# Kernel tuning notes

Measured on AMD Instinct MI355X. Metric: run time of the kernel, lower is better.

Reference implementation:

```python
import jax, jax.numpy as jnp
import numpy as np

EMBED = 768
FFN = 3072
HEADS = 12
HEAD_DIM = EMBED // HEADS
B, T = 4, 2048


def _layer_norm(x, g, b, eps=1e-5):
    m = jnp.mean(x, axis=-1, keepdims=True)
    v = jnp.mean((x - m) ** 2, axis=-1, keepdims=True)
    return (x - m) * jax.lax.rsqrt(v + eps) * g + b


def setup_inputs() -> dict:
    key = jax.random.key(0)
    ks = jax.random.split(key, 8)
    s_e = 1.0 / np.sqrt(EMBED)
    s_f = 1.0 / np.sqrt(FFN)
    # weights stored [in, out] (transpose of torch Linear layout)
    return {
        "x": jax.random.normal(ks[0], (B, T, EMBED), dtype=jnp.float32),
        "ln1_g": jnp.ones((EMBED,), jnp.float32),
        "ln1_b": jnp.zeros((EMBED,), jnp.float32),
        "wq": jax.random.uniform(ks[1], (EMBED, EMBED), jnp.float32, -s_e, s_e),
        "bq": jnp.zeros((EMBED,), jnp.float32),
        "wk": jax.random.uniform(ks[2], (EMBED, EMBED), jnp.float32, -s_e, s_e),
        "bk": jnp.zeros((EMBED,), jnp.float32),
        "wv": jax.random.uniform(ks[3], (EMBED, EMBED), jnp.float32, -s_e, s_e),
        "bv": jnp.zeros((EMBED,), jnp.float32),
        "wo": jax.random.uniform(ks[4], (EMBED, EMBED), jnp.float32, -s_e, s_e),
        "bo": jnp.zeros((EMBED,), jnp.float32),
        "ln2_g": jnp.ones((EMBED,), jnp.float32),
        "ln2_b": jnp.zeros((EMBED,), jnp.float32),
        "w1": jax.random.uniform(ks[5], (EMBED, FFN), jnp.float32, -s_e, s_e),
        "b1": jnp.zeros((FFN,), jnp.float32),
        "w2": jax.random.uniform(ks[6], (FFN, EMBED), jnp.float32, -s_f, s_f),
        "b2": jnp.zeros((EMBED,), jnp.float32),
    }


def reference(x, ln1_g, ln1_b, wq, bq, wk, bk, wv, bv, wo, bo,
              ln2_g, ln2_b, w1, b1, w2, b2):
    Bx, Tx, C = x.shape
    # --- self-attention block (pre-norm) ---
    residual = x
    h = _layer_norm(x, ln1_g, ln1_b)
    q = (h @ wq + bq).reshape(Bx, Tx, HEADS, HEAD_DIM)
    k = (h @ wk + bk).reshape(Bx, Tx, HEADS, HEAD_DIM)
    v = (h @ wv + bv).reshape(Bx, Tx, HEADS, HEAD_DIM)
    scale = 1.0 / np.sqrt(HEAD_DIM)
    attn = jnp.einsum('bqhd,bkhd->bhqk', q, k) * scale  # [B,H,T,T]
    attn = jax.nn.softmax(attn, axis=-1)
    o = jnp.einsum('bhqk,bkhd->bqhd', attn, v).reshape(Bx, Tx, C)
    x = residual + (o @ wo + bo)
    # --- FFN block (pre-norm) ---
    residual = x
    h = _layer_norm(x, ln2_g, ln2_b)
    h = jax.nn.gelu(h @ w1 + b1, approximate=False)
    x = residual + (h @ w2 + b2)
    return x
```

## Files before the change

kernel.cpp:

```cpp
#include <hip/hip_runtime.h>
#include <hip/hip_bf16.h>

#define EMBED 768
#define FFNDIM 3072
#define HEADS 12
#define HDIM  64
#define BB    4
#define TT    2048
#define MTOK  (BB*TT)

typedef __hip_bfloat16 bf16;
typedef __attribute__((ext_vector_type(8))) short short8;
typedef __attribute__((ext_vector_type(4))) float f32x4;
typedef __attribute__((ext_vector_type(16))) float f32x16;
typedef __attribute__((ext_vector_type(4))) unsigned short ushort4v;

__device__ __forceinline__ f32x4 mfma16(short8 a, short8 b, f32x4 c) {
  return __builtin_amdgcn_mfma_f32_16x16x32_bf16(a, b, c, 0, 0, 0);
}
__device__ __forceinline__ f32x16 mfma32(short8 a, short8 b, f32x16 c) {
  return __builtin_amdgcn_mfma_f32_32x32x16_bf16(a, b, c, 0, 0, 0);
}

__device__ __forceinline__ unsigned short f2bf(float f) {
  union { float f; unsigned int u; } v; v.f = f;
  unsigned int u = v.u;
  return (unsigned short)((u + 0x7fffu + ((u >> 16) & 1u)) >> 16);
}

__device__ __forceinline__ float fexp2(float x) {
#if __has_builtin(__builtin_amdgcn_exp2f)
  return __builtin_amdgcn_exp2f(x);
#else
  return exp2f(x);
#endif
}

__device__ __forceinline__ unsigned cvtpk(float lo, float hi) {
  unsigned r;
  asm("v_cvt_pk_bf16_f32 %0, %1, %2" : "=v"(r) : "v"(lo), "v"(hi));
  return r;
}
__device__ __forceinline__ void pl32swap(unsigned& vdst, unsigned& vsrc) {
  asm("v_permlane32_swap_b32 %0, %1" : "+v"(vdst), "+v"(vsrc));
}

__device__ __forceinline__ void gl_lds16(const void* g, void* l) {
  __builtin_amdgcn_global_load_lds((const __attribute__((address_space(1))) void*)g,
                                   (__attribute__((address_space(3))) void*)l, 16, 0, 0);
}

template <int N>
__device__ __forceinline__ void wait_vm() {
  asm volatile("s_waitcnt vmcnt(%0)" :: "i"(N) : "memory");
  __builtin_amdgcn_sched_barrier(0);
}
__device__ __forceinline__ void block_barrier() {
  __builtin_amdgcn_sched_barrier(0);
  __builtin_amdgcn_s_barrier();
  __builtin_amdgcn_sched_barrier(0);
}

#define QSCALE 0.18033688011112042f
#define DEFER_THR 11.54f

struct TArgs {
  const float* src[6];
  bf16* dst[6];
  int K[6];
  int N[6];
};

__global__ __launch_bounds__(256) void transpose_k(TArgs ta) {
  const int mi = blockIdx.z;
  const int K = ta.K[mi], N = ta.N[mi];
  const int nt = N / 32;
  const int bx = blockIdx.x % nt, by = blockIdx.x / nt;
  const int n0 = bx * 32, k0 = by * 32;
  if (k0 >= K) return;
  __shared__ float t[32][33];
  const float* __restrict__ W = ta.src[mi];
  bf16* __restrict__ Wt = ta.dst[mi];
  const int tx = threadIdx.x & 31, ty = threadIdx.x >> 5;
#pragma unroll
  for (int i = 0; i < 4; ++i) {
    int kk = ty + i * 8;
    t[tx][kk] = W[(size_t)(k0 + kk) * N + n0 + tx];
  }
  __syncthreads();
#pragma unroll
  for (int i = 0; i < 4; ++i) {
    int nn = ty + i * 8;
    Wt[(size_t)(n0 + nn) * K + k0 + tx] = __float2bfloat16(t[nn][tx]);
  }
}

__global__ __launch_bounds__(256) void ln_k(const float* __restrict__ x,
                                            const float* __restrict__ g,
                                            const float* __restrict__ b,
                                            bf16* __restrict__ out) {
  const int row = blockIdx.x * 4 + (threadIdx.x >> 6);
  const int lane = threadIdx.x & 63;
  const float* xr = x + (size_t)row * EMBED;
  float4 v[3];
  float s = 0.f;
#pragma unroll
  for (int i = 0; i < 3; ++i) {
    v[i] = *(const float4*)&xr[i * 256 + lane * 4];
    s += v[i].x + v[i].y + v[i].z + v[i].w;
  }
#pragma unroll
  for (int m = 1; m < 64; m <<= 1) s += __shfl_xor(s, m);
  const float mean = s * (1.f / 768.f);
  float ss = 0.f;
#pragma unroll
  for (int i = 0; i < 3; ++i) {
    float dx = v[i].x - mean, dy = v[i].y - mean, dz = v[i].z - mean, dw = v[i].w - mean;
    ss += dx * dx + dy * dy + dz * dz + dw * dw;
  }
#pragma unroll
  for (int m = 1; m < 64; m <<= 1) ss += __shfl_xor(ss, m);
  const float rstd = rsqrtf(ss * (1.f / 768.f) + 1e-5f);
#pragma unroll
  for (int i = 0; i < 3; ++i) {
    float4 g4 = *(const float4*)&g[i * 256 + lane * 4];
    float4 b4 = *(const float4*)&b[i * 256 + lane * 4];
    ushort4v o4;
    o4[0] = f2bf((v[i].x - mean) * rstd * g4.x + b4.x);
    o4[1] = f2bf((v[i].y - mean) * rstd * g4.y + b4.y);
    o4[2] = f2bf((v[i].z - mean) * rstd * g4.z + b4.z);
    o4[3] = f2bf((v[i].w - mean) * rstd * g4.w + b4.w);
    *(ushort4v*)&out[(size_t)row * EMBED + i * 256 + lane * 4] = o4;
  }
}

template <int EPI, int TN>
__global__ __launch_bounds__(256) void gemm_bt_k(
    const bf16* __restrict__ A, const bf16* __restrict__ Bt,
    const float* __restrict__ bias, const float* __restrict__ bias2,
    const float* __restrict__ bias3, const float* __restrict__ resid,
    float* __restrict__ outf, bf16* __restrict__ outb,
    bf16* __restrict__ outk, bf16* __restrict__ outvt,
    int N, int K) {
  constexpr int MI = (TN == 128) ? 4 : 2;
  constexpr int SN = (TN == 128) ? 4 : 3;
  const int tid = threadIdx.x;
  const int lane = tid & 63;
  const int w = tid >> 6;
  const int l16 = lane & 15, g = lane >> 4;
  const int wrbase = (TN == 128) ? (w >> 1) * 64 : w * 32;
  const int wcbase = (TN == 128) ? (w & 1) * 64 : 0;

  const int nbx = N / TN;
  const int logical = ((int)blockIdx.x & 7) * ((int)gridDim.x >> 3) + ((int)blockIdx.x >> 3);
  const int m0 = (logical / nbx) * 128, n0 = (logical % nbx) * TN;

  __shared__ bf16 Al[3][128 * 32];
  __shared__ bf16 Bl[3][TN * 32];

  f32x4 acc[MI][4];
#pragma unroll
  for (int i = 0; i < MI; ++i)
#pragma unroll
    for (int j = 0; j < 4; ++j) acc[i][j] = {0.f, 0.f, 0.f, 0.f};

  const int st_r = lane >> 2;
  const int st_c = ((lane & 3) ^ ((lane >> 3) & 3)) * 8;
  const size_t a_base = (size_t)(m0 + w * 32) * K;
  const size_t b_base = (TN == 128) ? (size_t)(n0 + w * 32) * K
                                    : (size_t)(n0 + w * 16) * K;

  auto stage = [&](int bufi, int kt) {
#pragma unroll
    for (int p = 0; p < 2; ++p)
      gl_lds16(A + a_base + (size_t)(p * 16 + st_r) * K + kt + st_c,
               &Al[bufi][(w * 32 + p * 16) * 32]);
    if constexpr (TN == 128) {
#pragma unroll
      for (int p = 0; p < 2; ++p)
        gl_lds16(Bt + b_base + (size_t)(p * 16 + st_r) * K + kt + st_c,
                 &Bl[bufi][(w * 32 + p * 16) * 32]);
    } else {
      gl_lds16(Bt + b_base + (size_t)st_r * K + kt + st_c, &Bl[bufi][(w * 16) * 32]);
    }
  };

  const int nt = K >> 5;
  stage(0, 0);
  stage(1, 32);
  const int sw = (l16 >> 1) & 3;
  int buf = 0;
  for (int t = 0; t < nt; ++t) {
    if (t < nt - 1) wait_vm<SN>(); else wait_vm<0>();
    block_barrier();
    if (t + 2 < nt) {
      int nb = buf + 2; if (nb >= 3) nb -= 3;
      stage(nb, (t + 2) * 32);
    }
    short8 af[MI], bfr[4];
#pragma unroll
    for (int i = 0; i < MI; ++i)
      af[i] = *(const short8*)&Al[buf][(wrbase + i * 16 + l16) * 32 + (g ^ sw) * 8];
#pragma unroll
    for (int j = 0; j < 4; ++j)
      bfr[j] = *(const short8*)&Bl[buf][(wcbase + j * 16 + l16) * 32 + (g ^ sw) * 8];
#pragma unroll
    for (int i = 0; i < MI; ++i)
#pragma unroll
      for (int j = 0; j < 4; ++j) acc[i][j] = mfma16(af[i], bfr[j], acc[i][j]);
    buf = (buf == 2) ? 0 : buf + 1;
  }

  const int crow = m0 + wrbase + g * 4;
  const int ccol = n0 + wcbase + l16;

  if constexpr (EPI == 0) {
    const int region = n0 / EMBED;
    const float* bp = (region == 0) ? bias : (region == 1) ? bias2 : bias3;
    if (region < 2) {
      const float sc = (region == 0) ? QSCALE : 1.0f;
      bf16* __restrict__ dst = (region == 0) ? outb : outk;
#pragma unroll
      for (int j = 0; j < 4; ++j) {
        const int cn = ccol - region * EMBED + j * 16;
        const float bvv = bp[cn];
#pragma unroll
        for (int i = 0; i < MI; ++i)
#pragma unroll
          for (int rr = 0; rr < 4; ++rr) {
            const int m = crow + i * 16 + rr;
            dst[(size_t)m * EMBED + cn] = __float2bfloat16((acc[i][j][rr] + bvv) * sc);
          }
      }
    } else {
#pragma unroll
      for (int j = 0; j < 4; ++j) {
        const int cn = ccol - 2 * EMBED + j * 16;
        const float bvv = bp[cn];
        const int hh = cn >> 6, dd = cn & 63;
#pragma unroll
        for (int i = 0; i < MI; ++i) {
          const int m = crow + i * 16;
          const int bb2 = m >> 11, t = m & 2047;
          ushort4v pk;
#pragma unroll
          for (int rr = 0; rr < 4; ++rr) pk[rr] = f2bf(acc[i][j][rr] + bvv);
          *(ushort4v*)&outvt[((size_t)((bb2 * HEADS + hh) * HDIM + dd)) * TT + t] = pk;
        }
      }
    }
  } else if constexpr (EPI == 1) {
#pragma unroll
    for (int j = 0; j < 4; ++j) {
      const int cn = ccol + j * 16;
      const float bvv = bias[cn];
#pragma unroll
      for (int i = 0; i < MI; ++i)
#pragma unroll
        for (int rr = 0; rr < 4; ++rr) {
          const int m = crow + i * 16 + rr;
          const size_t idx = (size_t)m * N + cn;
          outf[idx] = resid[idx] + acc[i][j][rr] + bvv;
        }
    }
  } else {
#pragma unroll
    for (int j = 0; j < 4; ++j) {
      const int cn = ccol + j * 16;
      const float bvv = bias[cn];
#pragma unroll
      for (int i = 0; i < MI; ++i)
#pragma unroll
        for (int rr = 0; rr < 4; ++rr) {
          const int m = crow + i * 16 + rr;
          const float v = acc[i][j][rr] + bvv;
          const float ge = 0.5f * v * (1.f + erff(v * 0.70710678118f));
          outb[(size_t)m * N + cn] = __float2bfloat16(ge);
        }
    }
  }
}

__global__ __launch_bounds__(256) void flash6_k(const bf16* __restrict__ q,
                                                const bf16* __restrict__ k,
                                                const bf16* __restrict__ vt,
                                                bf16* __restrict__ o) {
  const int tid = threadIdx.x, lane = tid & 63;
  const int l32 = lane & 31, hl = lane >> 5;
  const int w = tid >> 6;
  const int logical = ((int)blockIdx.x & 7) * 96 + ((int)blockIdx.x >> 3);
  const int qt = logical & 15;
  const int hb = logical >> 4;
  const int h = hb % HEADS, b = hb / HEADS;
  const int q0 = (qt * 4 + w) * 32;

  __shared__ bf16 Kl[3][64 * 64];
  __shared__ bf16 Vl[3][64 * 64];

  short8 qf[4];
  {
    const bf16* qp = q + (size_t)(b * TT + q0 + l32) * EMBED + h * HDIM + hl * 8;
#pragma unroll
    for (int c = 0; c < 4; ++c) qf[c] = *(const short8*)&qp[c * 16];
  }

  const bf16* __restrict__ kgs = k + (size_t)(b * TT) * EMBED + h * HDIM;
  const bf16* __restrict__ vgs = vt + ((size_t)((b * HEADS + h) * HDIM)) * TT;

  f32x16 oacc0, oacc1;
#pragma unroll
  for (int i = 0; i < 16; ++i) { oacc0[i] = 0.f; oacc1[i] = 0.f; }
  float mrun = -1.0e30f, lrun = 0.f;

  const int st_rw = w * 8 + (lane >> 3);
  const int st_cs0 = lane & 7;
  auto stage = [&](int buf, int kv) {
#pragma unroll
    for (int p = 0; p < 2; ++p) {
      const int r = p * 32 + st_rw;
      const int cs = st_cs0 ^ (r & 7);
      char* kdst = (char*)&Kl[buf][0] + p * 4096 + w * 1024;
      char* vdst = (char*)&Vl[buf][0] + p * 4096 + w * 1024;
      gl_lds16(kgs + (size_t)(kv + r) * EMBED + cs * 8, kdst);
      gl_lds16(vgs + (size_t)r * TT + kv + cs * 8, vdst);
    }
  };

  auto subtile = [&](int buf, int s2) {
    const int krow = s2 * 32 + l32;
    const char* Kb = (const char*)&Kl[buf][0];
    const char* Vb = (const char*)&Vl[buf][0];
    short8 kf[4];
#pragma unroll
    for (int c = 0; c < 4; ++c)
      kf[c] = *(const short8*)(Kb + krow * 128 + (((2 * c + hl) ^ (krow & 7)) * 16));

    f32x16 s;
#pragma unroll
    for (int i = 0; i < 16; ++i) s[i] = 0.f;
    __builtin_amdgcn_s_setprio(1);
#pragma unroll
    for (int c = 0; c < 4; ++c) s = mfma32(kf[c], qf[c], s);
    __builtin_amdgcn_s_setprio(0);

    short8 vf[4];
#pragma unroll
    for (int ks = 0; ks < 2; ++ks)
#pragma unroll
      for (int dc = 0; dc < 2; ++dc) {
        const int vrow = dc * 32 + l32;
        vf[ks * 2 + dc] = *(const short8*)(
            Vb + vrow * 128 + (((s2 * 4 + ks * 2 + hl) ^ (vrow & 7)) * 16));
      }

    float m0 = fmaxf(fmaxf(s[0], s[1]), s[2]);
    float m1 = fmaxf(fmaxf(s[3], s[4]), s[5]);
    float m2 = fmaxf(fmaxf(s[6], s[7]), s[8]);
    float m3 = fmaxf(fmaxf(s[9], s[10]), s[11]);
    float m4 = fmaxf(fmaxf(s[12], s[13]), s[14]);
    float mx = fmaxf(fmaxf(fmaxf(m0, m1), fmaxf(m2, m3)), fmaxf(m4, s[15]));
    mx = fmaxf(mx, __shfl_xor(mx, 32));

    if (!__all(mx <= mrun + DEFER_THR)) {
      const float mn = fmaxf(mrun, mx);
      const float al = fexp2(mrun - mn);
      lrun *= al;
#pragma unroll
      for (int i = 0; i < 16; ++i) { oacc0[i] *= al; oacc1[i] *= al; }
      mrun = mn;
    }

    float p[16];
#pragma unroll
    for (int i = 0; i < 16; ++i) p[i] = fexp2(s[i] - mrun);
    float a8[8];
#pragma unroll
    for (int i = 0; i < 8; ++i) a8[i] = p[2 * i] + p[2 * i + 1];
    float ps = ((a8[0] + a8[1]) + (a8[2] + a8[3])) + ((a8[4] + a8[5]) + (a8[6] + a8[7]));
    ps += __shfl_xor(ps, 32);
    lrun += ps;

    union { unsigned u[4]; short8 s8; } pa0, pa1;
    {
      unsigned U = cvtpk(p[0], p[1]), V = cvtpk(p[4], p[5]);
      pl32swap(V, U); pa0.u[0] = U; pa0.u[2] = V;
      unsigned U1 = cvtpk(p[2], p[3]), V1 = cvtpk(p[6], p[7]);
      pl32swap(V1, U1); pa0.u[1] = U1; pa0.u[3] = V1;
    }
    {
      unsigned U = cvtpk(p[8], p[9]), V = cvtpk(p[12], p[13]);
      pl32swap(V, U); pa1.u[0] = U; pa1.u[2] = V;
      unsigned U1 = cvtpk(p[10], p[11]), V1 = cvtpk(p[14], p[15]);
      pl32swap(V1, U1); pa1.u[1] = U1; pa1.u[3] = V1;
    }

    __builtin_amdgcn_s_setprio(1);
    oacc0 = mfma32(vf[0], pa0.s8, oacc0);
    oacc0 = mfma32(vf[2], pa1.s8, oacc0);
    oacc1 = mfma32(vf[1], pa0.s8, oacc1);
    oacc1 = mfma32(vf[3], pa1.s8, oacc1);
    __builtin_amdgcn_s_setprio(0);
  };

  const int NT = TT / 64;
  stage(0, 0);
  stage(1, 64);
  int buf = 0;
  for (int t = 0; t < NT; ++t) {
    if (t < NT - 1) wait_vm<4>(); else wait_vm<0>();
    block_barrier();
    if (t + 2 < NT) {
      int nb = buf + 2; if (nb >= 3) nb -= 3;
      stage(nb, (t + 2) * 64);
    }
    subtile(buf, 0);
    subtile(buf, 1);
    buf = (buf == 2) ? 0 : buf + 1;
  }

  const float inv = 1.f / lrun;
  bf16* op = o + (size_t)(b * TT + q0 + l32) * EMBED + h * HDIM;
#pragma unroll
  for (int a = 0; a < 4; ++a) {
    ushort4v pk4;
#pragma unroll
    for (int bb = 0; bb < 4; ++bb) pk4[bb] = f2bf(oacc0[a * 4 + bb] * inv);
    *(ushort4v*)&op[a * 8 + hl * 4] = pk4;
#pragma unroll
    for (int bb = 0; bb < 4; ++bb) pk4[bb] = f2bf(oacc1[a * 4 + bb] * inv);
    *(ushort4v*)&op[32 + a * 8 + hl * 4] = pk4;
  }
}

extern "C" void kernel_launch(void* const* d_in, const int* in_sizes, int n_in,
                              void* d_out, int out_size, void* d_ws,
                              size_t ws_size, hipStream_t stream) {
  const float* x = (const float*)d_in[0];
  const float* ln1g = (const float*)d_in[1];
  const float* ln1b = (const float*)d_in[2];
  const float* wq = (const float*)d_in[3];
  const float* bq = (const float*)d_in[4];
  const float* wk = (const float*)d_in[5];
  const float* bk = (const float*)d_in[6];
  const float* wv = (const float*)d_in[7];
  const float* bv = (const float*)d_in[8];
  const float* wo = (const float*)d_in[9];
  const float* bo = (const float*)d_in[10];
  const float* ln2g = (const float*)d_in[11];
  const float* ln2b = (const float*)d_in[12];
  const float* w1 = (const float*)d_in[13];
  const float* b1 = (const float*)d_in[14];
  const float* w2 = (const float*)d_in[15];
  const float* b2 = (const float*)d_in[16];
  float* out = (float*)d_out;

  char* ws = (char*)d_ws;
  size_t off = 0;
  auto alloc = [&](size_t bytes) {
    char* p = ws + off;
    off += (bytes + 255) & ~(size_t)255;
    return p;
  };
  bf16* wqkv_t = (bf16*)alloc((size_t)2304 * 768 * 2);
  bf16* wo_t = (bf16*)alloc((size_t)768 * 768 * 2);
  bf16* w1_t = (bf16*)alloc((size_t)3072 * 768 * 2);
  bf16* w2_t = (bf16*)alloc((size_t)768 * 3072 * 2);
  bf16* h = (bf16*)alloc((size_t)MTOK * EMBED * 2);
  char* qkvo = alloc((size_t)MTOK * EMBED * 2 * 4);
  bf16* qb = (bf16*)qkvo;
  bf16* kb = qb + (size_t)MTOK * EMBED;
  bf16* vtb = kb + (size_t)MTOK * EMBED;
  bf16* ob = vtb + (size_t)MTOK * EMBED;
  bf16* h1 = (bf16*)qkvo;
  float* x1 = (float*)alloc((size_t)MTOK * EMBED * 4);
  (void)ws_size;

  TArgs ta;
  ta.src[0] = wq; ta.dst[0] = wqkv_t;                  ta.K[0] = 768;  ta.N[0] = 768;
  ta.src[1] = wk; ta.dst[1] = wqkv_t + 768 * 768;      ta.K[1] = 768;  ta.N[1] = 768;
  ta.src[2] = wv; ta.dst[2] = wqkv_t + 2 * 768 * 768;  ta.K[2] = 768;  ta.N[2] = 768;
  ta.src[3] = wo; ta.dst[3] = wo_t;                    ta.K[3] = 768;  ta.N[3] = 768;
  ta.src[4] = w1; ta.dst[4] = w1_t;                    ta.K[4] = 768;  ta.N[4] = 3072;
  ta.src[5] = w2; ta.dst[5] = w2_t;                    ta.K[5] = 3072; ta.N[5] = 768;

  transpose_k<<<dim3(2304, 1, 6), dim3(256), 0, stream>>>(ta);
  ln_k<<<dim3(MTOK / 4), dim3(256), 0, stream>>>(x, ln1g, ln1b, h);
  gemm_bt_k<0, 128><<<dim3((2304 / 128) * (MTOK / 128)), dim3(256), 0, stream>>>(
      h, wqkv_t, bq, bk, bv, nullptr, nullptr, qb, kb, vtb, 2304, 768);
  flash6_k<<<dim3(16 * HEADS * BB), dim3(256), 0, stream>>>(qb, kb, vtb, ob);
  gemm_bt_k<1, 64><<<dim3((768 / 64) * (MTOK / 128)), dim3(256), 0, stream>>>(
      ob, wo_t, bo, nullptr, nullptr, x, x1, nullptr, nullptr, nullptr, 768, 768);
  ln_k<<<dim3(MTOK / 4), dim3(256), 0, stream>>>(x1, ln2g, ln2b, h);
  gemm_bt_k<2, 128><<<dim3((3072 / 128) * (MTOK / 128)), dim3(256), 0, stream>>>(
      h, w1_t, b1, nullptr, nullptr, nullptr, nullptr, h1, nullptr, nullptr, 3072, 768);
  gemm_bt_k<1, 64><<<dim3((768 / 64) * (MTOK / 128)), dim3(256), 0, stream>>>(
      h1, w2_t, b2, nullptr, nullptr, x1, out, nullptr, nullptr, nullptr, 768, 3072);
}
```

Baseline: 314.6 us.

## Split attention KV range in two halves and merge with a combine kernel

Splits each attention query tile's KV sequence into two halves processed by separate blocks (split-K flash attention). Each block writes unnormalized bf16 partial outputs plus running max and sum, and a new combine kernel merges the two halves with rescaling. V is now read directly from global memory instead of being staged in LDS, and K staging drops from triple to double buffering with full barriers. This doubles the grid for better occupancy, at the cost of an extra kernel, extra partial-output traffic, bf16 rounding of the unnormalized partials, and uncached V loads.

```diff
diff --git a/kernel.cpp b/kernel.cpp
--- a/kernel.cpp
+++ b/kernel.cpp
@@ -281,21 +281,24 @@
   }
 }
 
-__global__ __launch_bounds__(256) void flash6_k(const bf16* __restrict__ q,
+__global__ __launch_bounds__(256) void flash7_k(const bf16* __restrict__ q,
                                                 const bf16* __restrict__ k,
                                                 const bf16* __restrict__ vt,
-                                                bf16* __restrict__ o) {
+                                                bf16* __restrict__ po,
+                                                float2* __restrict__ ml) {
   const int tid = threadIdx.x, lane = tid & 63;
   const int l32 = lane & 31, hl = lane >> 5;
   const int w = tid >> 6;
-  const int logical = ((int)blockIdx.x & 7) * 96 + ((int)blockIdx.x >> 3);
+  const int logical = ((int)blockIdx.x & 7) * 192 + ((int)blockIdx.x >> 3);
   const int qt = logical & 15;
-  const int hb = logical >> 4;
+  const int rest = logical >> 4;
+  const int half = rest & 1;
+  const int hb = rest >> 1;
   const int h = hb % HEADS, b = hb / HEADS;
   const int q0 = (qt * 4 + w) * 32;
-
-  __shared__ bf16 Kl[3][64 * 64];
-  __shared__ bf16 Vl[3][64 * 64];
+  const int kv0 = half * (TT / 2);
+
+  __shared__ bf16 Kl[2][64 * 64];
 
   short8 qf[4];
   {
@@ -319,22 +322,27 @@
     for (int p = 0; p < 2; ++p) {
       const int r = p * 32 + st_rw;
       const int cs = st_cs0 ^ (r & 7);
-      char* kdst = (char*)&Kl[buf][0] + p * 4096 + w * 1024;
-      char* vdst = (char*)&Vl[buf][0] + p * 4096 + w * 1024;
-      gl_lds16(kgs + (size_t)(kv + r) * EMBED + cs * 8, kdst);
-      gl_lds16(vgs + (size_t)r * TT + kv + cs * 8, vdst);
+      gl_lds16(kgs + (size_t)(kv + r) * EMBED + cs * 8,
+               (char*)&Kl[buf][0] + p * 4096 + w * 1024);
     }
   };
 
-  auto subtile = [&](int buf, int s2) {
+  auto subtile = [&](int buf, int kvabs, int s2) {
     const int krow = s2 * 32 + l32;
     const char* Kb = (const char*)&Kl[buf][0];
-    const char* Vb = (const char*)&Vl[buf][0];
     short8 kf[4];
 #pragma unroll
     for (int c = 0; c < 4; ++c)
       kf[c] = *(const short8*)(Kb + krow * 128 + (((2 * c + hl) ^ (krow & 7)) * 16));
 
+    short8 vf[4];
+#pragma unroll
+    for (int ks = 0; ks < 2; ++ks)
+#pragma unroll
+      for (int dc = 0; dc < 2; ++dc)
+        vf[ks * 2 + dc] = *(const short8*)&vgs[(size_t)(dc * 32 + l32) * TT +
+                                               kvabs + ks * 16 + hl * 8];
+
     f32x16 s;
 #pragma unroll
     for (int i = 0; i < 16; ++i) s[i] = 0.f;
@@ -342,16 +350,6 @@
 #pragma unroll
     for (int c = 0; c < 4; ++c) s = mfma32(kf[c], qf[c], s);
     __builtin_amdgcn_s_setprio(0);
-
-    short8 vf[4];
-#pragma unroll
-    for (int ks = 0; ks < 2; ++ks)
-#pragma unroll
-      for (int dc = 0; dc < 2; ++dc) {
-        const int vrow = dc * 32 + l32;
-        vf[ks * 2 + dc] = *(const short8*)(
-            Vb + vrow * 128 + (((s2 * 4 + ks * 2 + hl) ^ (vrow & 7)) * 16));
-      }
 
     float m0 = fmaxf(fmaxf(s[0], s[1]), s[2]);
     float m1 = fmaxf(fmaxf(s[3], s[4]), s[5]);
@@ -402,34 +400,53 @@
     __builtin_amdgcn_s_setprio(0);
   };
 
-  const int NT = TT / 64;
-  stage(0, 0);
-  stage(1, 64);
+  const int NT = (TT / 2) / 64;
+  stage(0, kv0);
+  __syncthreads();
   int buf = 0;
   for (int t = 0; t < NT; ++t) {
-    if (t < NT - 1) wait_vm<4>(); else wait_vm<0>();
-    block_barrier();
-    if (t + 2 < NT) {
-      int nb = buf + 2; if (nb >= 3) nb -= 3;
-      stage(nb, (t + 2) * 64);
-    }
-    subtile(buf, 0);
-    subtile(buf, 1);
-    buf = (buf == 2) ? 0 : buf + 1;
-  }
-
-  const float inv = 1.f / lrun;
-  bf16* op = o + (size_t)(b * TT + q0 + l32) * EMBED + h * HDIM;
+    if (t + 1 < NT) stage(buf ^ 1, kv0 + (t + 1) * 64);
+    subtile(buf, kv0 + t * 64, 0);
+    subtile(buf, kv0 + t * 64 + 32, 1);
+    __syncthreads();
+    buf ^= 1;
+  }
+
+  bf16* pp = po + ((size_t)((half * BB + b) * HEADS + h) * TT + q0 + l32) * 64;
 #pragma unroll
   for (int a = 0; a < 4; ++a) {
     ushort4v pk4;
 #pragma unroll
-    for (int bb = 0; bb < 4; ++bb) pk4[bb] = f2bf(oacc0[a * 4 + bb] * inv);
-    *(ushort4v*)&op[a * 8 + hl * 4] = pk4;
-#pragma unroll
-    for (int bb = 0; bb < 4; ++bb) pk4[bb] = f2bf(oacc1[a * 4 + bb] * inv);
-    *(ushort4v*)&op[32 + a * 8 + hl * 4] = pk4;
-  }
+    for (int bb = 0; bb < 4; ++bb) pk4[bb] = f2bf(oacc0[a * 4 + bb]);
+    *(ushort4v*)&pp[a * 8 + hl * 4] = pk4;
+#pragma unroll
+    for (int bb = 0; bb < 4; ++bb) pk4[bb] = f2bf(oacc1[a * 4 + bb]);
+    *(ushort4v*)&pp[32 + a * 8 + hl * 4] = pk4;
+  }
+  if (hl == 0) {
+    float2 v2; v2.x = mrun; v2.y = lrun;
+    ml[(size_t)((half * BB + b) * HEADS + h) * TT + q0 + l32] = v2;
+  }
+}
+
+__global__ __launch_bounds__(256) void combine_k(const bf16* __restrict__ po,
+                                                 const float2* __restrict__ ml,
+                                                 bf16* __restrict__ o) {
+  const int row = blockIdx.x * 4 + (threadIdx.x >> 6);
+  const int lane = threadIdx.x & 63;
+  const size_t NR = (size_t)BB * HEADS * TT;
+  const float2 a = ml[row];
+  const float2 c = ml[NR + row];
+  const float M = fmaxf(a.x, c.x);
+  const float w0 = fexp2(a.x - M), w1 = fexp2(c.x - M);
+  const float inv = 1.f / (w0 * a.y + w1 * c.y);
+  const float o0 = __bfloat162float(po[(size_t)row * 64 + lane]);
+  const float o1 = __bfloat162float(po[NR * 64 + (size_t)row * 64 + lane]);
+  const float val = (w0 * o0 + w1 * o1) * inv;
+  const int b = row / (HEADS * TT);
+  const int rem = row % (HEADS * TT);
+  const int h = rem / TT, t = rem % TT;
+  o[((size_t)(b * TT + t)) * EMBED + h * HDIM + lane] = __float2bfloat16(val);
 }
 
 extern "C" void kernel_launch(void* const* d_in, const int* in_sizes, int n_in,
@@ -474,6 +491,8 @@
   bf16* h1 = (bf16*)qkvo;
   float* x1 = (float*)alloc((size_t)MTOK * EMBED * 4);
   (void)ws_size;
+  bf16* po = (bf16*)x1;
+  float2* mlb = (float2*)h;
 
   TArgs ta;
   ta.src[0] = wq; ta.dst[0] = wqkv_t;                  ta.K[0] = 768;  ta.N[0] = 768;
@@ -487,7 +506,8 @@
   ln_k<<<dim3(MTOK / 4), dim3(256), 0, stream>>>(x, ln1g, ln1b, h);
   gemm_bt_k<0, 128><<<dim3((2304 / 128) * (MTOK / 128)), dim3(256), 0, stream>>>(
       h, wqkv_t, bq, bk, bv, nullptr, nullptr, qb, kb, vtb, 2304, 768);
-  flash6_k<<<dim3(16 * HEADS * BB), dim3(256), 0, stream>>>(qb, kb, vtb, ob);
+  flash7_k<<<dim3(16 * HEADS * BB * 2), dim3(256), 0, stream>>>(qb, kb, vtb, po, mlb);
+  combine_k<<<dim3(BB * HEADS * TT / 4), dim3(256), 0, stream>>>(po, mlb, ob);
   gemm_bt_k<1, 64><<<dim3((768 / 64) * (MTOK / 128)), dim3(256), 0, stream>>>(
       ob, wo_t, bo, nullptr, nullptr, x, x1, nullptr, nullptr, nullptr, 768, 768);
   ln_k<<<dim3(MTOK / 4), dim3(256), 0, stream>>>(x1, ln2g, ln2b, h);
```

New measurement: 355.9 us. 1.13x slower.
